# Performance work log

Hardware: AMD Instinct MI355X
Metric: run time of the kernel (lower is better)

## Reference

```python
import jax, jax.numpy as jnp
import numpy as np

NUM_HEADS = 16

def setup_inputs() -> dict:
    key = jax.random.key(0)
    k1, k2, k3 = jax.random.split(key, 3)
    D = 1024
    return {
        "hidden_states": jax.random.normal(k1, (2, 2048, D), dtype=jnp.float32),
        "c_attn_w": jax.random.normal(k2, (D, 3 * D), dtype=jnp.float32) * 0.02,
        "c_attn_b": jnp.zeros((3 * D,), dtype=jnp.float32),
        "c_proj_w": jax.random.normal(k3, (D, D), dtype=jnp.float32) * 0.02,
        "c_proj_b": jnp.zeros((D,), dtype=jnp.float32),
    }

def reference(hidden_states, c_attn_w, c_attn_b, c_proj_w, c_proj_b):
    B, S, D = hidden_states.shape
    H = NUM_HEADS
    hd = D // H
    # Conv1D: x @ W + b, then split into q, k, v
    qkv = hidden_states @ c_attn_w + c_attn_b  # [B, S, 3D]
    q, k, v = jnp.split(qkv, 3, axis=-1)
    q = q.reshape(B, S, H, hd).transpose(0, 2, 1, 3)  # [B, H, S, hd]
    k = k.reshape(B, S, H, hd).transpose(0, 2, 1, 3)
    v = v.reshape(B, S, H, hd).transpose(0, 2, 1, 3)
    # scaled QK^T
    scores = jnp.einsum("bhqd,bhkd->bhqk", q, k) / jnp.asarray(hd ** 0.5, q.dtype)
    # causal mask (tril), masked positions set to dtype min per original code
    causal = jnp.tril(jnp.ones((S, S), dtype=bool))
    mask_value = jnp.finfo(scores.dtype).min
    scores = jnp.where(causal[None, None], scores, mask_value)
    attn = jax.nn.softmax(scores, axis=-1)
    out = jnp.einsum("bhqk,bhkd->bhqd", attn, v)  # [B, H, S, hd]
    out = out.transpose(0, 2, 1, 3).reshape(B, S, D)
    out = out @ c_proj_w + c_proj_b
    return out
```

## Files before the change

kernel.cpp:

```cpp
#include <hip/hip_runtime.h>
#include <hip/hip_bf16.h>
#include <math.h>

#define B_ 2
#define S_ 2048
#define D_ 1024
#define H_ 16
#define HD 64
#define M_ (B_ * S_)
#define N_QKV (3 * D_)
#define LOG2E_8 0.18033688011112042f

typedef short short8 __attribute__((ext_vector_type(8)));
typedef float floatx4 __attribute__((ext_vector_type(4)));

static __device__ __forceinline__ unsigned short f2bf(float x) {
    __hip_bfloat16 h = __float2bfloat16(x);
    unsigned short u;
    __builtin_memcpy(&u, &h, sizeof(u));
    return u;
}
static __device__ __forceinline__ float bf2f(unsigned short b) {
    union { unsigned u; float f; } v; v.u = ((unsigned)b) << 16;
    return v.f;
}
static __device__ __forceinline__ void split2(float x, unsigned short& h, unsigned short& l) {
    h = f2bf(x);
    l = f2bf(x - bf2f(h));
}

static __device__ __forceinline__ void dma16(const void* g, void* l) {
    __builtin_amdgcn_global_load_lds(
        (const __attribute__((address_space(1))) unsigned int*)g,
        (__attribute__((address_space(3))) unsigned int*)l,
        16, 0, 0);
}

__global__ __launch_bounds__(256) void prep_all(
    const float* __restrict__ hs,
    const float* __restrict__ attn_w,
    const float* __restrict__ proj_w,
    unsigned short* __restrict__ Ahi, unsigned short* __restrict__ Alo,
    unsigned short* __restrict__ WqThi, unsigned short* __restrict__ WqTlo,
    unsigned short* __restrict__ WpThi, unsigned short* __restrict__ WpTlo)
{
    __shared__ float Ws[64][68];
    const int bid = blockIdx.x;
    const int t   = threadIdx.x;

    if (bid < 2048) {
        const size_t i = ((size_t)bid * 256 + t) * 8;
        float4 a = *(const float4*)(hs + i);
        float4 b = *(const float4*)(hs + i + 4);
        float xs[8] = {a.x, a.y, a.z, a.w, b.x, b.y, b.z, b.w};
        short8 h, l;
#pragma unroll
        for (int e = 0; e < 8; e++) {
            unsigned short hh, ll;
            split2(xs[e], hh, ll);
            h[e] = (short)hh; l[e] = (short)ll;
        }
        *(short8*)&Ahi[i] = h;
        *(short8*)&Alo[i] = l;
        return;
    }

    const float* W; unsigned short *Thi, *Tlo; int N, n0, k0;
    if (bid < 2816) {
        const int s = bid - 2048;
        W = attn_w; Thi = WqThi; Tlo = WqTlo; N = N_QKV;
        n0 = (s % 48) * 64; k0 = (s / 48) * 64;
    } else {
        const int s = bid - 2816;
        W = proj_w; Thi = WpThi; Tlo = WpTlo; N = D_;
        n0 = (s % 16) * 64; k0 = (s / 16) * 64;
    }
    {
        const int kl = t >> 4, nl = (t & 15) * 4;
        const float* src = W + (size_t)(k0 + kl) * N + n0 + nl;
#pragma unroll
        for (int g = 0; g < 4; g++)
            *(float4*)&Ws[kl + g * 16][nl] = *(const float4*)(src + (size_t)g * 16 * N);
    }
    __syncthreads();
    {
        const int nl = t >> 2, ks = (t & 3) * 16;
        short8 h0, h1, l0, l1;
#pragma unroll
        for (int j = 0; j < 8; j++) {
            unsigned short hh, ll;
            split2(Ws[ks + j][nl], hh, ll);
            h0[j] = (short)hh; l0[j] = (short)ll;
        }
#pragma unroll
        for (int j = 0; j < 8; j++) {
            unsigned short hh, ll;
            split2(Ws[ks + 8 + j][nl], hh, ll);
            h1[j] = (short)hh; l1[j] = (short)ll;
        }
        unsigned short* dh = Thi + (size_t)(n0 + nl) * D_ + k0 + ks;
        unsigned short* dl = Tlo + (size_t)(n0 + nl) * D_ + k0 + ks;
        *(short8*)dh = h0; *(short8*)(dh + 8) = h1;
        *(short8*)dl = l0; *(short8*)(dl + 8) = l1;
    }
}

__global__ __launch_bounds__(256) void gemm_qkv(
    const unsigned short* __restrict__ Ahi, const unsigned short* __restrict__ Alo,
    const unsigned short* __restrict__ BThi, const unsigned short* __restrict__ BTlo,
    const float* __restrict__ bias,
    unsigned short* __restrict__ Qhi, unsigned short* __restrict__ Qlo,
    unsigned short* __restrict__ Khi, unsigned short* __restrict__ Klo,
    unsigned short* __restrict__ vThi, unsigned short* __restrict__ vTlo)
{
    __shared__ unsigned short sAh[128 * 32], sAl[128 * 32];
    __shared__ unsigned short sBh[128 * 32], sBl[128 * 32];

    const int t    = threadIdx.x;
    const int m0   = blockIdx.y * 128, n0 = blockIdx.x * 128;
    const int lane = t & 63, wave = t >> 6;
    const int lm   = lane & 15, quad = lane >> 4;
    const int wm   = (wave >> 1) * 64, wn = (wave & 1) * 64;

    const int lrow = lane >> 2, lcol = (lane & 3) * 8;
    const unsigned short* gAh = Ahi + (size_t)(m0 + wave * 32 + lrow) * D_ + lcol;
    const unsigned short* gAl = Alo + (size_t)(m0 + wave * 32 + lrow) * D_ + lcol;
    const unsigned short* gBh = BThi + (size_t)(n0 + wave * 32 + lrow) * D_ + lcol;
    const unsigned short* gBl = BTlo + (size_t)(n0 + wave * 32 + lrow) * D_ + lcol;
    const int ldst = wave * 1024 + lane * 8;

    floatx4 acc[4][4];
#pragma unroll
    for (int i = 0; i < 4; i++)
#pragma unroll
        for (int j = 0; j < 4; j++)
#pragma unroll
            for (int r = 0; r < 4; r++) acc[i][j][r] = 0.f;

    for (int k0 = 0; k0 < D_; k0 += 32) {
        __syncthreads();
        dma16(gAh + k0, &sAh[ldst]);
        dma16(gAh + (size_t)16 * D_ + k0, &sAh[ldst + 512]);
        dma16(gAl + k0, &sAl[ldst]);
        dma16(gAl + (size_t)16 * D_ + k0, &sAl[ldst + 512]);
        dma16(gBh + k0, &sBh[ldst]);
        dma16(gBh + (size_t)16 * D_ + k0, &sBh[ldst + 512]);
        dma16(gBl + k0, &sBl[ldst]);
        dma16(gBl + (size_t)16 * D_ + k0, &sBl[ldst + 512]);
        __syncthreads();

        short8 bhf[4], blf[4];
#pragma unroll
        for (int nb = 0; nb < 4; nb++) {
            const int r = wn + nb * 16 + lm;
            bhf[nb] = *(const short8*)&sBh[r * 32 + quad * 8];
            blf[nb] = *(const short8*)&sBl[r * 32 + quad * 8];
        }
#pragma unroll
        for (int mb = 0; mb < 4; mb++) {
            const int r = wm + mb * 16 + lm;
            short8 ah = *(const short8*)&sAh[r * 32 + quad * 8];
            short8 al = *(const short8*)&sAl[r * 32 + quad * 8];
#pragma unroll
            for (int nb = 0; nb < 4; nb++) {
                acc[mb][nb] = __builtin_amdgcn_mfma_f32_16x16x32_bf16(ah, bhf[nb], acc[mb][nb], 0, 0, 0);
                acc[mb][nb] = __builtin_amdgcn_mfma_f32_16x16x32_bf16(al, bhf[nb], acc[mb][nb], 0, 0, 0);
                acc[mb][nb] = __builtin_amdgcn_mfma_f32_16x16x32_bf16(ah, blf[nb], acc[mb][nb], 0, 0, 0);
            }
        }
    }

    const int nmode = n0 >> 10;
    if (nmode == 0) {
#pragma unroll
        for (int nb = 0; nb < 4; nb++) {
            const int c = n0 + wn + nb * 16 + lm;
            const float bv = bias[c];
#pragma unroll
            for (int mb = 0; mb < 4; mb++) {
                const int rowb = m0 + wm + mb * 16 + quad * 4;
#pragma unroll
                for (int r = 0; r < 4; r++) {
                    unsigned short hh, ll;
                    split2((acc[mb][nb][r] + bv) * LOG2E_8, hh, ll);
                    Qhi[(size_t)(rowb + r) * D_ + c] = hh;
                    Qlo[(size_t)(rowb + r) * D_ + c] = ll;
                }
            }
        }
    } else if (nmode == 1) {
#pragma unroll
        for (int nb = 0; nb < 4; nb++) {
            const int c = n0 + wn + nb * 16 + lm;
            const float bv = bias[c];
            const int cq = c - 1024;
#pragma unroll
            for (int mb = 0; mb < 4; mb++) {
                const int rowb = m0 + wm + mb * 16 + quad * 4;
#pragma unroll
                for (int r = 0; r < 4; r++) {
                    unsigned short hh, ll;
                    split2(acc[mb][nb][r] + bv, hh, ll);
                    Khi[(size_t)(rowb + r) * D_ + cq] = hh;
                    Klo[(size_t)(rowb + r) * D_ + cq] = ll;
                }
            }
        }
    } else {
#pragma unroll
        for (int nb = 0; nb < 4; nb++) {
            const int c = n0 + wn + nb * 16 + lm;
            const float bv = bias[c];
            const int cq = c - 2048;
            const int hh_ = cq >> 6, dd = cq & 63;
#pragma unroll
            for (int mb = 0; mb < 4; mb++) {
                const int rowb = m0 + wm + mb * 16 + quad * 4;
                const int bb = rowb >> 11, ss = rowb & 2047;
                unsigned short hv[4], lv[4];
#pragma unroll
                for (int r = 0; r < 4; r++)
                    split2(acc[mb][nb][r] + bv, hv[r], lv[r]);
                const size_t idx = ((size_t)((bb * 16 + hh_) * 64 + dd)) * S_ + ss;
                *(uint2*)&vThi[idx] = make_uint2((unsigned)hv[0] | ((unsigned)hv[1] << 16),
                                                 (unsigned)hv[2] | ((unsigned)hv[3] << 16));
                *(uint2*)&vTlo[idx] = make_uint2((unsigned)lv[0] | ((unsigned)lv[1] << 16),
                                                 (unsigned)lv[2] | ((unsigned)lv[3] << 16));
            }
        }
    }
}

__global__ __launch_bounds__(256) void gemm_out(
    const unsigned short* __restrict__ Ahi, const unsigned short* __restrict__ Alo,
    const unsigned short* __restrict__ BThi, const unsigned short* __restrict__ BTlo,
    const float* __restrict__ bias, float* __restrict__ C)
{
    __shared__ unsigned short sAh[64 * 64], sAl[64 * 64];
    __shared__ unsigned short sBh[64 * 64], sBl[64 * 64];

    const int t   = threadIdx.x;
    const int lid = blockIdx.x;
    const int swz = (lid & 7) * 128 + (lid >> 3);
    const int bx  = swz & 15, by = swz >> 4;
    const int m0  = by * 64, n0 = bx * 64;
    const int lane = t & 63, wave = t >> 6;
    const int lm   = lane & 15, quad = lane >> 4;

    const int r0   = t >> 3;
    const int gseg = (t & 7) ^ (r0 & 7);
    const unsigned short* gAh = Ahi + (size_t)(m0 + r0) * D_ + gseg * 8;
    const unsigned short* gAl = Alo + (size_t)(m0 + r0) * D_ + gseg * 8;
    const unsigned short* gBh = BThi + (size_t)(n0 + r0) * D_ + gseg * 8;
    const unsigned short* gBl = BTlo + (size_t)(n0 + r0) * D_ + gseg * 8;
    const int ld0  = t * 8;
    const int swzr = lm & 7;

    floatx4 acc[4];
#pragma unroll
    for (int j = 0; j < 4; j++)
#pragma unroll
        for (int r = 0; r < 4; r++) acc[j][r] = 0.f;

    for (int k0 = 0; k0 < D_; k0 += 64) {
        __syncthreads();
        dma16(gAh + k0, &sAh[ld0]);
        dma16(gAh + (size_t)32 * D_ + k0, &sAh[ld0 + 2048]);
        dma16(gAl + k0, &sAl[ld0]);
        dma16(gAl + (size_t)32 * D_ + k0, &sAl[ld0 + 2048]);
        dma16(gBh + k0, &sBh[ld0]);
        dma16(gBh + (size_t)32 * D_ + k0, &sBh[ld0 + 2048]);
        dma16(gBl + k0, &sBl[ld0]);
        dma16(gBl + (size_t)32 * D_ + k0, &sBl[ld0 + 2048]);
        __syncthreads();

#pragma unroll
        for (int ks = 0; ks < 2; ks++) {
            const int arow = (wave * 16 + lm) * 64 + (((ks * 4 + quad) ^ swzr) * 8);
            short8 ah = *(const short8*)&sAh[arow];
            short8 al = *(const short8*)&sAl[arow];
#pragma unroll
            for (int nb = 0; nb < 4; nb++) {
                const int brow = (nb * 16 + lm) * 64 + (((ks * 4 + quad) ^ swzr) * 8);
                short8 bh = *(const short8*)&sBh[brow];
                short8 bl = *(const short8*)&sBl[brow];
                acc[nb] = __builtin_amdgcn_mfma_f32_16x16x32_bf16(ah, bh, acc[nb], 0, 0, 0);
                acc[nb] = __builtin_amdgcn_mfma_f32_16x16x32_bf16(al, bh, acc[nb], 0, 0, 0);
                acc[nb] = __builtin_amdgcn_mfma_f32_16x16x32_bf16(ah, bl, acc[nb], 0, 0, 0);
            }
        }
    }

#pragma unroll
    for (int nb = 0; nb < 4; nb++) {
        const int col = n0 + nb * 16 + lm;
        const float bv = bias[col];
#pragma unroll
        for (int r = 0; r < 4; r++) {
            const int row = m0 + wave * 16 + quad * 4 + r;
            C[(size_t)row * D_ + col] = acc[nb][r] + bv;
        }
    }
}

#define PSP 72

__global__ __launch_bounds__(512, 4) void flash_attn_mfma(
    unsigned short* QAhi, unsigned short* QAlo,
    const unsigned short* __restrict__ Khi, const unsigned short* __restrict__ Klo,
    const unsigned short* __restrict__ vThi, const unsigned short* __restrict__ vTlo)
{
    __shared__ unsigned short KhS[64 * 64], KlS[64 * 64];
    __shared__ unsigned short VhS[64 * 64], VlS[64 * 64];
    __shared__ unsigned short PhS[128 * PSP], PlS[128 * PSP];

    const int t    = threadIdx.x;
    const int lid  = blockIdx.x + 16 * blockIdx.y;
    const int bh   = (lid & 7) * 4 + ((lid >> 3) & 3);
    const int pj   = lid >> 5;
    const int b    = bh >> 4, h = bh & 15;
    const int lane = t & 63, w = t >> 6;
    const int lm   = lane & 15, quad = lane >> 4;

    const int qt = (bh & 1) ? (15 - pj) : pj;
    const int q0 = qt * 128;
    const int ntiles = 2 * qt + 2;
    const int wdiag = (q0 >> 6) + (w >> 2);

    const int r0  = t >> 3;
    const int seg = (t & 7) ^ (r0 & 7);
    const unsigned short* gKh = Khi + (size_t)(b * S_ + r0) * D_ + h * HD + 8 * seg;
    const unsigned short* gKl = Klo + (size_t)(b * S_ + r0) * D_ + h * HD + 8 * seg;
    const unsigned short* gVh = vThi + ((size_t)((b * 16 + h) * 64 + r0)) * S_ + 8 * seg;
    const unsigned short* gVl = vTlo + ((size_t)((b * 16 + h) * 64 + r0)) * S_ + 8 * seg;
    const int ld0 = t * 8;
    const int swzr = (lm & 7) << 3;

    short8 qh[2], ql[2];
    {
        const size_t qoff = (size_t)(b * S_ + q0 + 16 * w + lm) * D_ + h * HD + quad * 8;
        qh[0] = *(const short8*)&QAhi[qoff];
        qh[1] = *(const short8*)&QAhi[qoff + 32];
        ql[0] = *(const short8*)&QAlo[qoff];
        ql[1] = *(const short8*)&QAlo[qoff + 32];
    }

    float lsum[4] = {0.f, 0.f, 0.f, 0.f};
    floatx4 o[4];
#pragma unroll
    for (int nb = 0; nb < 4; nb++)
#pragma unroll
        for (int r = 0; r < 4; r++) o[nb][r] = 0.f;

    for (int kt = 0; kt < ntiles; kt++) {
        __syncthreads();
        {
            const size_t ko = (size_t)(kt * 64) * D_;
            const int vo = kt * 64;
            dma16(gKh + ko, &KhS[ld0]);
            dma16(gKl + ko, &KlS[ld0]);
            dma16(gVh + vo, &VhS[ld0]);
            dma16(gVl + vo, &VlS[ld0]);
        }
        __syncthreads();

        if (kt <= wdiag) {
            floatx4 sa[4];
#pragma unroll
            for (int nb = 0; nb < 4; nb++)
#pragma unroll
                for (int r = 0; r < 4; r++) sa[nb][r] = 0.f;
            __builtin_amdgcn_s_setprio(1);
#pragma unroll
            for (int s = 0; s < 2; s++) {
#pragma unroll
                for (int nb = 0; nb < 4; nb++) {
                    const int ka = (nb * 16 + lm) * 64 + ((s * 32 + quad * 8) ^ swzr);
                    short8 kh = *(const short8*)&KhS[ka];
                    short8 kl = *(const short8*)&KlS[ka];
                    sa[nb] = __builtin_amdgcn_mfma_f32_16x16x32_bf16(qh[s], kh, sa[nb], 0, 0, 0);
                    sa[nb] = __builtin_amdgcn_mfma_f32_16x16x32_bf16(ql[s], kh, sa[nb], 0, 0, 0);
                    sa[nb] = __builtin_amdgcn_mfma_f32_16x16x32_bf16(qh[s], kl, sa[nb], 0, 0, 0);
                }
            }
            __builtin_amdgcn_s_setprio(0);

            const bool diag = (kt == wdiag);
            const int kbase = kt * 64;
#pragma unroll
            for (int r = 0; r < 4; r++) {
                const int qabs = q0 + 16 * w + 4 * quad + r;
                const int rloc = 16 * w + 4 * quad + r;
#pragma unroll
                for (int nb = 0; nb < 4; nb++) {
                    float p = exp2f(sa[nb][r]);
                    if (diag && (kbase + 16 * nb + lm > qabs)) p = 0.f;
                    lsum[r] += p;
                    unsigned short hh, ll;
                    split2(p, hh, ll);
                    PhS[rloc * PSP + 16 * nb + lm] = hh;
                    PlS[rloc * PSP + 16 * nb + lm] = ll;
                }
            }

            __builtin_amdgcn_s_setprio(1);
#pragma unroll
            for (int ks = 0; ks < 2; ks++) {
                short8 pf = *(const short8*)&PhS[(16 * w + lm) * PSP + ks * 32 + quad * 8];
                short8 pg = *(const short8*)&PlS[(16 * w + lm) * PSP + ks * 32 + quad * 8];
#pragma unroll
                for (int nb = 0; nb < 4; nb++) {
                    const int va = (nb * 16 + lm) * 64 + ((ks * 32 + quad * 8) ^ swzr);
                    short8 vhf = *(const short8*)&VhS[va];
                    short8 vlf = *(const short8*)&VlS[va];
                    o[nb] = __builtin_amdgcn_mfma_f32_16x16x32_bf16(pf, vhf, o[nb], 0, 0, 0);
                    o[nb] = __builtin_amdgcn_mfma_f32_16x16x32_bf16(pg, vhf, o[nb], 0, 0, 0);
                    o[nb] = __builtin_amdgcn_mfma_f32_16x16x32_bf16(pf, vlf, o[nb], 0, 0, 0);
                }
            }
            __builtin_amdgcn_s_setprio(0);
        }
    }

#pragma unroll
    for (int r = 0; r < 4; r++) {
        float l = lsum[r];
        l += __shfl_xor(l, 1);
        l += __shfl_xor(l, 2);
        l += __shfl_xor(l, 4);
        l += __shfl_xor(l, 8);
        const float inv = 1.f / l;
        const size_t rowoff =
            (size_t)(b * S_ + q0 + 16 * w + 4 * quad + r) * D_ + h * HD + lm;
#pragma unroll
        for (int nb = 0; nb < 4; nb++) {
            unsigned short hh, ll;
            split2(o[nb][r] * inv, hh, ll);
            QAhi[rowoff + 16 * nb] = hh;
            QAlo[rowoff + 16 * nb] = ll;
        }
    }
}

extern "C" void kernel_launch(void* const* d_in, const int* in_sizes, int n_in,
                              void* d_out, int out_size, void* d_ws, size_t ws_size,
                              hipStream_t stream)
{
    const float* hs     = (const float*)d_in[0];
    const float* attn_w = (const float*)d_in[1];
    const float* attn_b = (const float*)d_in[2];
    const float* proj_w = (const float*)d_in[3];
    const float* proj_b = (const float*)d_in[4];
    float* outp = (float*)d_out;

    const size_t QE = (size_t)M_ * D_;
    const size_t WQ = (size_t)D_ * N_QKV;
    unsigned short* Qhi   = (unsigned short*)d_ws;
    unsigned short* Qlo   = Qhi + QE;
    unsigned short* Khi   = Qlo + QE;
    unsigned short* Klo   = Khi + QE;
    unsigned short* vThi  = Klo + QE;
    unsigned short* vTlo  = vThi + QE;
    unsigned short* WqThi = vTlo + QE;
    unsigned short* WqTlo = WqThi + WQ;
    unsigned short* WpThi = WqTlo + WQ;
    unsigned short* WpTlo = WpThi + (size_t)D_ * D_;
    unsigned short* Ahi   = WpTlo + (size_t)D_ * D_;
    unsigned short* Alo   = Ahi + QE;

    dim3 blk(256);
    prep_all<<<dim3(3072), blk, 0, stream>>>(
        hs, attn_w, proj_w, Ahi, Alo, WqThi, WqTlo, WpThi, WpTlo);
    gemm_qkv<<<dim3(N_QKV / 128, M_ / 128), blk, 0, stream>>>(
        Ahi, Alo, WqThi, WqTlo, attn_b, Qhi, Qlo, Khi, Klo, vThi, vTlo);
    flash_attn_mfma<<<dim3(16, B_ * H_), dim3(512), 0, stream>>>(
        Qhi, Qlo, Khi, Klo, vThi, vTlo);
    gemm_out<<<dim3(1024), blk, 0, stream>>>(
        Qhi, Qlo, WpThi, WpTlo, proj_b, outp);
}
```

Baseline: 299.1 us.

## Triple-buffer QKV GEMM shared tiles and use 512-thread blocks

Rewrites the QKV projection GEMM's main loop to use a 3-stage shared-memory ring with async DMA loads issued two k-tiles ahead. Each step waits on vmcnt and uses a single barrier instead of two __syncthreads per iteration. The block grows from 256 to 512 threads (8 waves, each computing a 32x64 sub-tile), which halves per-wave accumulators and raises occupancy. Shared memory use rises to 96KB per block, which may limit how many blocks fit per CU.

```diff
diff --git a/kernel.cpp b/kernel.cpp
--- a/kernel.cpp
+++ b/kernel.cpp
@@ -105,7 +105,7 @@
     }
 }
 
-__global__ __launch_bounds__(256) void gemm_qkv(
+__global__ __launch_bounds__(512, 2) void gemm_qkv(
     const unsigned short* __restrict__ Ahi, const unsigned short* __restrict__ Alo,
     const unsigned short* __restrict__ BThi, const unsigned short* __restrict__ BTlo,
     const float* __restrict__ bias,
@@ -113,54 +113,59 @@
     unsigned short* __restrict__ Khi, unsigned short* __restrict__ Klo,
     unsigned short* __restrict__ vThi, unsigned short* __restrict__ vTlo)
 {
-    __shared__ unsigned short sAh[128 * 32], sAl[128 * 32];
-    __shared__ unsigned short sBh[128 * 32], sBl[128 * 32];
+    __shared__ unsigned short S[3][4][128 * 32];
 
     const int t    = threadIdx.x;
     const int m0   = blockIdx.y * 128, n0 = blockIdx.x * 128;
     const int lane = t & 63, wave = t >> 6;
     const int lm   = lane & 15, quad = lane >> 4;
-    const int wm   = (wave >> 1) * 64, wn = (wave & 1) * 64;
-
-    const int lrow = lane >> 2, lcol = (lane & 3) * 8;
-    const unsigned short* gAh = Ahi + (size_t)(m0 + wave * 32 + lrow) * D_ + lcol;
-    const unsigned short* gAl = Alo + (size_t)(m0 + wave * 32 + lrow) * D_ + lcol;
-    const unsigned short* gBh = BThi + (size_t)(n0 + wave * 32 + lrow) * D_ + lcol;
-    const unsigned short* gBl = BTlo + (size_t)(n0 + wave * 32 + lrow) * D_ + lcol;
-    const int ldst = wave * 1024 + lane * 8;
-
-    floatx4 acc[4][4];
-#pragma unroll
-    for (int i = 0; i < 4; i++)
+    const int wm   = (wave >> 1) * 32, wn = (wave & 1) * 64;
+
+    const int srow = t >> 2, scol = (t & 3) * 8;
+    const unsigned short* gAh = Ahi + (size_t)(m0 + srow) * D_ + scol;
+    const unsigned short* gAl = Alo + (size_t)(m0 + srow) * D_ + scol;
+    const unsigned short* gBh = BThi + (size_t)(n0 + srow) * D_ + scol;
+    const unsigned short* gBl = BTlo + (size_t)(n0 + srow) * D_ + scol;
+    const int ld = t * 8;
+
+#define STAGE_QKV(BUF, K0)                          \
+    { dma16(gAh + (K0), &S[BUF][0][ld]);            \
+      dma16(gAl + (K0), &S[BUF][1][ld]);            \
+      dma16(gBh + (K0), &S[BUF][2][ld]);            \
+      dma16(gBl + (K0), &S[BUF][3][ld]); }
+
+    floatx4 acc[2][4];
+#pragma unroll
+    for (int i = 0; i < 2; i++)
 #pragma unroll
         for (int j = 0; j < 4; j++)
 #pragma unroll
             for (int r = 0; r < 4; r++) acc[i][j][r] = 0.f;
 
-    for (int k0 = 0; k0 < D_; k0 += 32) {
-        __syncthreads();
-        dma16(gAh + k0, &sAh[ldst]);
-        dma16(gAh + (size_t)16 * D_ + k0, &sAh[ldst + 512]);
-        dma16(gAl + k0, &sAl[ldst]);
-        dma16(gAl + (size_t)16 * D_ + k0, &sAl[ldst + 512]);
-        dma16(gBh + k0, &sBh[ldst]);
-        dma16(gBh + (size_t)16 * D_ + k0, &sBh[ldst + 512]);
-        dma16(gBl + k0, &sBl[ldst]);
-        dma16(gBl + (size_t)16 * D_ + k0, &sBl[ldst + 512]);
-        __syncthreads();
+    STAGE_QKV(0, 0);
+    STAGE_QKV(1, 32);
+    asm volatile("s_waitcnt vmcnt(4)" ::: "memory");
+    __builtin_amdgcn_s_barrier();
+
+    int buf = 0;
+    for (int kt = 0; kt < 32; kt++) {
+        if (kt + 2 < 32) {
+            const int nb2 = (buf + 2 >= 3) ? (buf - 1) : (buf + 2);
+            STAGE_QKV(nb2, (kt + 2) * 32);
+        }
 
         short8 bhf[4], blf[4];
 #pragma unroll
         for (int nb = 0; nb < 4; nb++) {
-            const int r = wn + nb * 16 + lm;
-            bhf[nb] = *(const short8*)&sBh[r * 32 + quad * 8];
-            blf[nb] = *(const short8*)&sBl[r * 32 + quad * 8];
-        }
-#pragma unroll
-        for (int mb = 0; mb < 4; mb++) {
-            const int r = wm + mb * 16 + lm;
-            short8 ah = *(const short8*)&sAh[r * 32 + quad * 8];
-            short8 al = *(const short8*)&sAl[r * 32 + quad * 8];
+            const int r = (wn + nb * 16 + lm) * 32 + quad * 8;
+            bhf[nb] = *(const short8*)&S[buf][2][r];
+            blf[nb] = *(const short8*)&S[buf][3][r];
+        }
+#pragma unroll
+        for (int mb = 0; mb < 2; mb++) {
+            const int r = (wm + mb * 16 + lm) * 32 + quad * 8;
+            short8 ah = *(const short8*)&S[buf][0][r];
+            short8 al = *(const short8*)&S[buf][1][r];
 #pragma unroll
             for (int nb = 0; nb < 4; nb++) {
                 acc[mb][nb] = __builtin_amdgcn_mfma_f32_16x16x32_bf16(ah, bhf[nb], acc[mb][nb], 0, 0, 0);
@@ -168,7 +173,13 @@
                 acc[mb][nb] = __builtin_amdgcn_mfma_f32_16x16x32_bf16(ah, blf[nb], acc[mb][nb], 0, 0, 0);
             }
         }
-    }
+
+        if (kt + 2 < 32) asm volatile("s_waitcnt vmcnt(4)" ::: "memory");
+        else             asm volatile("s_waitcnt vmcnt(0)" ::: "memory");
+        __builtin_amdgcn_s_barrier();
+        buf = (buf + 1 >= 3) ? 0 : (buf + 1);
+    }
+#undef STAGE_QKV
 
     const int nmode = n0 >> 10;
     if (nmode == 0) {
@@ -177,7 +188,7 @@
             const int c = n0 + wn + nb * 16 + lm;
             const float bv = bias[c];
 #pragma unroll
-            for (int mb = 0; mb < 4; mb++) {
+            for (int mb = 0; mb < 2; mb++) {
                 const int rowb = m0 + wm + mb * 16 + quad * 4;
 #pragma unroll
                 for (int r = 0; r < 4; r++) {
@@ -195,7 +206,7 @@
             const float bv = bias[c];
             const int cq = c - 1024;
 #pragma unroll
-            for (int mb = 0; mb < 4; mb++) {
+            for (int mb = 0; mb < 2; mb++) {
                 const int rowb = m0 + wm + mb * 16 + quad * 4;
 #pragma unroll
                 for (int r = 0; r < 4; r++) {
@@ -214,7 +225,7 @@
             const int cq = c - 2048;
             const int hh_ = cq >> 6, dd = cq & 63;
 #pragma unroll
-            for (int mb = 0; mb < 4; mb++) {
+            for (int mb = 0; mb < 2; mb++) {
                 const int rowb = m0 + wm + mb * 16 + quad * 4;
                 const int bb = rowb >> 11, ss = rowb & 2047;
                 unsigned short hv[4], lv[4];
@@ -471,7 +482,7 @@
     dim3 blk(256);
     prep_all<<<dim3(3072), blk, 0, stream>>>(
         hs, attn_w, proj_w, Ahi, Alo, WqThi, WqTlo, WpThi, WpTlo);
-    gemm_qkv<<<dim3(N_QKV / 128, M_ / 128), blk, 0, stream>>>(
+    gemm_qkv<<<dim3(N_QKV / 128, M_ / 128), dim3(512), 0, stream>>>(
         Ahi, Alo, WqThi, WqTlo, attn_b, Qhi, Qlo, Khi, Klo, vThi, vTlo);
     flash_attn_mfma<<<dim3(16, B_ * H_), dim3(512), 0, stream>>>(
         Qhi, Qlo, Khi, Klo, vThi, vTlo);
```

Result: slower. 307.4 us (+2.8%).
